# Optimization experiments

Measured on AMD Instinct MI355X. Metric: run time of the kernel, lower is better.

Reference implementation:

```python
import jax, jax.numpy as jnp
import numpy as np

VOCAB = 100000
DIM = 300
B = 65536
K = 10


def setup_inputs() -> dict:
    key = jax.random.key(0)
    k1, k2, k3, k4 = jax.random.split(key, 4)
    initrange = 1.0 / DIM
    u_weight = jax.random.uniform(k1, (VOCAB, DIM), jnp.float32, -initrange, initrange)
    v_weight = jnp.zeros((VOCAB, DIM), jnp.float32)
    pos_u = jax.random.randint(k2, (B,), 0, VOCAB)
    pos_v = jax.random.randint(k3, (B,), 0, VOCAB)
    neg_v = jax.random.randint(k4, (B, K), 0, VOCAB)
    return {"u_weight": u_weight, "v_weight": v_weight,
            "pos_u": pos_u, "pos_v": pos_v, "neg_v": neg_v}


def reference(u_weight, v_weight, pos_u, pos_v, neg_v):
    emb_u = u_weight[pos_u]          # [B, D]
    emb_v = v_weight[pos_v]          # [B, D]
    emb_neg_v = v_weight[neg_v]      # [B, K, D]

    score = jnp.sum(emb_u * emb_v, axis=1)               # [B]
    score = jnp.clip(score, -10.0, 10.0)
    pos_loss = -jax.nn.log_sigmoid(score)                # [B]

    neg_score = jnp.einsum('bkd,bd->bk', emb_neg_v, emb_u)  # [B, K]
    neg_score = jnp.clip(neg_score, -10.0, 10.0)
    neg_loss = -jnp.sum(jax.nn.log_sigmoid(-neg_score), axis=1)  # [B]

    return jnp.mean(pos_loss + neg_loss)
```

## Files before the change

### kernel.cpp

```cpp
#include <hip/hip_runtime.h>
#include <math.h>


#define DIM   300
#define B_TOT 65536
#define K_NEG 10
#define NROW  (K_NEG + 2)

constexpr int BLOCKS = 4096;
constexpr int TPB    = 256;
constexpr int WAVES  = BLOCKS * (TPB / 64);
constexpr int B_PER_WAVE = B_TOT / WAVES;

typedef float vf4 __attribute__((ext_vector_type(4)));

__device__ __forceinline__ float dot4(vf4 a, vf4 b) {
    vf4 p = a * b;
    return p.x + p.y + p.z + p.w;
}

__device__ __forceinline__ vf4 ld_nt(const vf4* p) {
    return __builtin_nontemporal_load(p);
}

__global__
__attribute__((amdgpu_flat_work_group_size(256, 256)))
__attribute__((amdgpu_waves_per_eu(4, 4)))
void sg_main(
    const float* __restrict__ uw, const float* __restrict__ vw,
    const int* __restrict__ pos_u, const int* __restrict__ pos_v,
    const int* __restrict__ neg_v, float* __restrict__ block_sums)
{
    const int lane = threadIdx.x & 63;
    const int wib  = threadIdx.x >> 6;
    int gw = blockIdx.x * (TPB / 64) + wib;
    gw = __builtin_amdgcn_readfirstlane(gw);

    const bool c1ok = lane < (75 - 64);
    const int  o2   = c1ok ? (64 + lane) : lane;

    const int b0 = gw * B_PER_WAVE;

    int idx[B_PER_WAVE][NROW];
    #pragma unroll
    for (int i = 0; i < B_PER_WAVE; ++i) {
        idx[i][0] = __builtin_amdgcn_readfirstlane(pos_u[b0 + i]);
        idx[i][1] = __builtin_amdgcn_readfirstlane(pos_v[b0 + i]);
        #pragma unroll
        for (int k = 0; k < K_NEG; ++k)
            idx[i][2 + k] = __builtin_amdgcn_readfirstlane(neg_v[(b0 + i) * K_NEG + k]);
    }

    vf4 c0[NROW];
    vf4 c1[NROW];

    auto issue = [&](int i) {
        {
            const vf4* bu = (const vf4*)(uw + (size_t)idx[i][0] * DIM);
            c0[0] = ld_nt(bu + lane);
            c1[0] = ld_nt(bu + o2);
        }
        #pragma unroll
        for (int j = 1; j < NROW; ++j) {
            const vf4* bv = (const vf4*)(vw + (size_t)idx[i][j] * DIM);
            c0[j] = bv[lane];
            c1[j] = bv[o2];
        }
    };

    issue(0);

    float acc = 0.f;

    #pragma unroll
    for (int i = 0; i < B_PER_WAVE; ++i) {
        float part[K_NEG + 1];
        #pragma unroll
        for (int j = 1; j < NROW; ++j) {
            float p = dot4(c0[j], c0[0]);
            float q = dot4(c1[j], c1[0]);
            part[j - 1] = p + (c1ok ? q : 0.f);
        }

        if (i + 1 < B_PER_WAVE) issue(i + 1);
        __builtin_amdgcn_sched_barrier(0x7);

        #pragma unroll
        for (int s = 1; s < 64; s <<= 1) {
            #pragma unroll
            for (int j = 0; j < K_NEG + 1; ++j)
                part[j] += __shfl_xor(part[j], s, 64);
        }

        float score = fminf(fmaxf(part[0], -10.f), 10.f);
        float loss = __logf(1.f + __expf(-score));
        #pragma unroll
        for (int k = 0; k < K_NEG; ++k) {
            float ns = fminf(fmaxf(part[k + 1], -10.f), 10.f);
            loss += __logf(1.f + __expf(ns));
        }
        acc += loss;
    }

    __shared__ float red[TPB / 64];
    if (lane == 0) red[wib] = acc;
    __syncthreads();
    if (threadIdx.x == 0)
        block_sums[blockIdx.x] = red[0] + red[1] + red[2] + red[3];
}

__global__ __launch_bounds__(256) void sg_finalize(
    const float* __restrict__ bs, float* __restrict__ out)
{
    float s = 0.f;
    for (int i = threadIdx.x; i < BLOCKS; i += 256) s += bs[i];
    #pragma unroll
    for (int off = 1; off < 64; off <<= 1) s += __shfl_xor(s, off, 64);
    __shared__ float red[4];
    const int wave = threadIdx.x >> 6;
    if ((threadIdx.x & 63) == 0) red[wave] = s;
    __syncthreads();
    if (threadIdx.x == 0)
        out[0] = (red[0] + red[1] + red[2] + red[3]) * (1.0f / (float)B_TOT);
}

extern "C" void kernel_launch(void* const* d_in, const int* in_sizes, int n_in,
                              void* d_out, int out_size, void* d_ws, size_t ws_size,
                              hipStream_t stream) {
    const float* uw    = (const float*)d_in[0];
    const float* vw    = (const float*)d_in[1];
    const int*   pos_u = (const int*)d_in[2];
    const int*   pos_v = (const int*)d_in[3];
    const int*   neg_v = (const int*)d_in[4];
    float* out = (float*)d_out;
    float* block_sums = (float*)d_ws;

    sg_main<<<BLOCKS, TPB, 0, stream>>>(uw, vw, pos_u, pos_v, neg_v, block_sums);
    sg_finalize<<<1, 256, 0, stream>>>(block_sums, out);
}
```

Before: 344.5 us.

## Assign one batch element per wave and drop in-wave software prefetch

Each wave now handles a single batch element instead of four, so the grid grows to 16384 blocks. The manual prefetch of the next element's rows and the fixed waves-per-EU attribute are removed, leaving the hardware to hide gather latency through more resident waves. This trades explicit pipelining for more parallelism, at the cost of more block launches and more partial sums for the finalize kernel to read.

```diff
diff --git a/kernel.cpp b/kernel.cpp
--- a/kernel.cpp
+++ b/kernel.cpp
@@ -7,10 +7,9 @@
 #define K_NEG 10
 #define NROW  (K_NEG + 2)
 
-constexpr int BLOCKS = 4096;
 constexpr int TPB    = 256;
-constexpr int WAVES  = BLOCKS * (TPB / 64);
-constexpr int B_PER_WAVE = B_TOT / WAVES;
+constexpr int WPB    = TPB / 64;
+constexpr int BLOCKS = B_TOT / WPB;
 
 typedef float vf4 __attribute__((ext_vector_type(4)));
 
@@ -23,87 +22,67 @@
     return __builtin_nontemporal_load(p);
 }
 
-__global__
-__attribute__((amdgpu_flat_work_group_size(256, 256)))
-__attribute__((amdgpu_waves_per_eu(4, 4)))
-void sg_main(
+__global__ __launch_bounds__(TPB) void sg_main(
     const float* __restrict__ uw, const float* __restrict__ vw,
     const int* __restrict__ pos_u, const int* __restrict__ pos_v,
     const int* __restrict__ neg_v, float* __restrict__ block_sums)
 {
     const int lane = threadIdx.x & 63;
     const int wib  = threadIdx.x >> 6;
-    int gw = blockIdx.x * (TPB / 64) + wib;
+    int gw = blockIdx.x * WPB + wib;
     gw = __builtin_amdgcn_readfirstlane(gw);
 
     const bool c1ok = lane < (75 - 64);
     const int  o2   = c1ok ? (64 + lane) : lane;
 
-    const int b0 = gw * B_PER_WAVE;
+    const int b = gw;
 
-    int idx[B_PER_WAVE][NROW];
+    int idx[NROW];
+    idx[0] = __builtin_amdgcn_readfirstlane(pos_u[b]);
+    idx[1] = __builtin_amdgcn_readfirstlane(pos_v[b]);
     #pragma unroll
-    for (int i = 0; i < B_PER_WAVE; ++i) {
-        idx[i][0] = __builtin_amdgcn_readfirstlane(pos_u[b0 + i]);
-        idx[i][1] = __builtin_amdgcn_readfirstlane(pos_v[b0 + i]);
-        #pragma unroll
-        for (int k = 0; k < K_NEG; ++k)
-            idx[i][2 + k] = __builtin_amdgcn_readfirstlane(neg_v[(b0 + i) * K_NEG + k]);
-    }
+    for (int k = 0; k < K_NEG; ++k)
+        idx[2 + k] = __builtin_amdgcn_readfirstlane(neg_v[b * K_NEG + k]);
 
     vf4 c0[NROW];
     vf4 c1[NROW];
+    {
+        const vf4* bu = (const vf4*)(uw + (size_t)idx[0] * DIM);
+        c0[0] = ld_nt(bu + lane);
+        c1[0] = ld_nt(bu + o2);
+    }
+    #pragma unroll
+    for (int j = 1; j < NROW; ++j) {
+        const vf4* bv = (const vf4*)(vw + (size_t)idx[j] * DIM);
+        c0[j] = bv[lane];
+        c1[j] = bv[o2];
+    }
 
-    auto issue = [&](int i) {
-        {
-            const vf4* bu = (const vf4*)(uw + (size_t)idx[i][0] * DIM);
-            c0[0] = ld_nt(bu + lane);
-            c1[0] = ld_nt(bu + o2);
-        }
-        #pragma unroll
-        for (int j = 1; j < NROW; ++j) {
-            const vf4* bv = (const vf4*)(vw + (size_t)idx[i][j] * DIM);
-            c0[j] = bv[lane];
-            c1[j] = bv[o2];
-        }
-    };
-
-    issue(0);
-
-    float acc = 0.f;
+    float part[K_NEG + 1];
+    #pragma unroll
+    for (int j = 1; j < NROW; ++j) {
+        float p = dot4(c0[j], c0[0]);
+        float q = dot4(c1[j], c1[0]);
+        part[j - 1] = p + (c1ok ? q : 0.f);
+    }
 
     #pragma unroll
-    for (int i = 0; i < B_PER_WAVE; ++i) {
-        float part[K_NEG + 1];
+    for (int s = 1; s < 64; s <<= 1) {
         #pragma unroll
-        for (int j = 1; j < NROW; ++j) {
-            float p = dot4(c0[j], c0[0]);
-            float q = dot4(c1[j], c1[0]);
-            part[j - 1] = p + (c1ok ? q : 0.f);
-        }
-
-        if (i + 1 < B_PER_WAVE) issue(i + 1);
-        __builtin_amdgcn_sched_barrier(0x7);
-
-        #pragma unroll
-        for (int s = 1; s < 64; s <<= 1) {
-            #pragma unroll
-            for (int j = 0; j < K_NEG + 1; ++j)
-                part[j] += __shfl_xor(part[j], s, 64);
-        }
-
-        float score = fminf(fmaxf(part[0], -10.f), 10.f);
-        float loss = __logf(1.f + __expf(-score));
-        #pragma unroll
-        for (int k = 0; k < K_NEG; ++k) {
-            float ns = fminf(fmaxf(part[k + 1], -10.f), 10.f);
-            loss += __logf(1.f + __expf(ns));
-        }
-        acc += loss;
+        for (int j = 0; j < K_NEG + 1; ++j)
+            part[j] += __shfl_xor(part[j], s, 64);
     }
 
-    __shared__ float red[TPB / 64];
-    if (lane == 0) red[wib] = acc;
+    float score = fminf(fmaxf(part[0], -10.f), 10.f);
+    float loss = __logf(1.f + __expf(-score));
+    #pragma unroll
+    for (int k = 0; k < K_NEG; ++k) {
+        float ns = fminf(fmaxf(part[k + 1], -10.f), 10.f);
+        loss += __logf(1.f + __expf(ns));
+    }
+
+    __shared__ float red[WPB];
+    if (lane == 0) red[wib] = loss;
     __syncthreads();
     if (threadIdx.x == 0)
         block_sums[blockIdx.x] = red[0] + red[1] + red[2] + red[3];
```

After: 350.6 us. Within noise of the previous version (+1.8%).
